# Optimization experiments

Measured on AMD Instinct MI355X. Metric: run time of the kernel, lower is better.

## Reference

```python
import jax, jax.numpy as jnp
import numpy as np

D_MODEL = 96
D_INNER = 192        # expand_factor * d_model
D_STATE = 16
DT_RANK = 6          # ceil(d_model / 16)
D_CONV = 4
N_LAYERS = 2
EPS = 1e-5


def conv3d(x, w, b=None, padding=((0, 0), (0, 0), (0, 0)), groups=1):
    # x: (N, C, L, H, W), w: (O, C//groups, kL, kH, kW)
    y = jax.lax.conv_general_dilated(
        x, w, window_strides=(1, 1, 1), padding=padding,
        dimension_numbers=('NCDHW', 'OIDHW', 'NCDHW'),
        feature_group_count=groups)
    return y if b is None else y + b[None, :, None, None, None]


def rmsnorm(x, w):
    # faithful to source: mean of squares over the LAST dim (W)
    return x * jax.lax.rsqrt(jnp.mean(x * x, axis=-1, keepdims=True) + EPS) * w


def mamba_block(x, p):
    # x: (N, d_model, L, H, W)
    L = x.shape[2]
    xz = conv3d(x, p['in_proj_w'], padding=((0, 0), (1, 1), (1, 1)))
    xi, z = xz[:, :D_INNER], xz[:, D_INNER:]
    # causal depthwise temporal conv: pad d_conv-1, crop to L
    xi = conv3d(xi, p['conv1d_w'], p['conv1d_b'],
                padding=((D_CONV - 1, D_CONV - 1), (0, 0), (0, 0)),
                groups=D_INNER)[:, :, :L]
    xi = jax.nn.silu(xi)
    # --- SSM (selective scan, pscan path) ---
    A = -jnp.exp(p['A_log'])                                   # (K, S)
    dbc = conv3d(xi, p['x_proj_w'])                            # (N, dt_rank+2S, L, H, W)
    delta = jax.nn.softplus(conv3d(dbc[:, :DT_RANK], p['dt_proj_w'], p['dt_proj_b']))  # (N, K, L, H, W)
    B = jnp.moveaxis(dbc[:, DT_RANK:DT_RANK + D_STATE], 1, -1)  # (N, L, H, W, S)
    C = dbc[:, DT_RANK + D_STATE:]                              # (N, S, L, H, W)
    deltaA = jnp.exp(delta[..., None] * A[None, :, None, None, None, :])  # (N,K,L,H,W,S)
    BX = delta[..., None] * B[:, None] * xi[..., None]                    # (N,K,L,H,W,S)

    def op(e1, e2):
        a1, b1 = e1
        a2, b2 = e2
        return a1 * a2, a2 * b1 + b2

    _, hs = jax.lax.associative_scan(op, (deltaA, BX), axis=2)  # scan over L
    y = jnp.einsum('nklhws,nslhw->nklhw', hs, C) + p['D'][None, :, None, None, None] * xi
    out = y * jax.nn.silu(z)
    return conv3d(out, p['out_proj_w'])


def _forward(x, in_proj_w, conv1d_w, conv1d_b, x_proj_w, dt_proj_w,
             dt_proj_b, A_log, D, out_proj_w, norm_w):
    for l in range(N_LAYERS):
        p = dict(in_proj_w=in_proj_w[l], conv1d_w=conv1d_w[l], conv1d_b=conv1d_b[l],
                 x_proj_w=x_proj_w[l], dt_proj_w=dt_proj_w[l], dt_proj_b=dt_proj_b[l],
                 A_log=A_log[l], D=D[l], out_proj_w=out_proj_w[l], norm_w=norm_w[l])
        x = mamba_block(rmsnorm(x, p['norm_w']), p) + x   # ResidualBlock
        x = x[:, :, 0:1]                                   # Mamba.forward keeps t=0 only
    return x


def setup_inputs() -> dict:
    key = jax.random.key(0)
    ks = jax.random.split(key, 12)
    Lk = N_LAYERS
    x = jax.random.normal(ks[0], (2, D_MODEL, 8, 24, 24), dtype=jnp.float32)
    in_proj_w = jax.random.normal(ks[1], (Lk, 2 * D_INNER, D_MODEL, 1, 3, 3), jnp.float32) * (D_MODEL * 9) ** -0.5
    conv1d_w = jax.random.normal(ks[2], (Lk, D_INNER, 1, D_CONV, 1, 1), jnp.float32) * D_CONV ** -0.5
    conv1d_b = jax.random.normal(ks[3], (Lk, D_INNER), jnp.float32) * 0.02
    x_proj_w = jax.random.normal(ks[4], (Lk, DT_RANK + 2 * D_STATE, D_INNER, 1, 1, 1), jnp.float32) * D_INNER ** -0.5
    dt_std = DT_RANK ** -0.5
    dt_proj_w = jax.random.uniform(ks[5], (Lk, D_INNER, DT_RANK, 1, 1, 1), jnp.float32, -dt_std, dt_std)
    # dt bias init: inv softplus of dt ~ LogUniform(dt_min, dt_max)
    dt = jnp.exp(jax.random.uniform(ks[6], (Lk, D_INNER), jnp.float32)
                 * (np.log(0.1) - np.log(0.001)) + np.log(0.001))
    dt = jnp.clip(dt, 1e-4, None)
    dt_proj_b = dt + jnp.log(-jnp.expm1(-dt))
    A_log = jnp.log(jnp.tile(jnp.arange(1, D_STATE + 1, dtype=jnp.float32), (Lk, D_INNER, 1)))
    D = jnp.ones((Lk, D_INNER), jnp.float32)
    out_proj_w = jax.random.normal(ks[7], (Lk, D_MODEL, D_INNER, 1, 1, 1), jnp.float32) * D_INNER ** -0.5
    norm_w = jnp.ones((Lk, 1, D_MODEL, 1, 1, 1), jnp.float32)
    return {'x': x, 'in_proj_w': in_proj_w, 'conv1d_w': conv1d_w, 'conv1d_b': conv1d_b,
            'x_proj_w': x_proj_w, 'dt_proj_w': dt_proj_w, 'dt_proj_b': dt_proj_b,
            'A_log': A_log, 'D': D, 'out_proj_w': out_proj_w, 'norm_w': norm_w}


def reference(x, in_proj_w, conv1d_w, conv1d_b, x_proj_w, dt_proj_w,
              dt_proj_b, A_log, D, out_proj_w, norm_w):
    return _forward(x, in_proj_w, conv1d_w, conv1d_b, x_proj_w, dt_proj_w,
                    dt_proj_b, A_log, D, out_proj_w, norm_w)
```

## Files before the change

### kernel.cpp

```cpp
#include <hip/hip_runtime.h>
#include <math.h>

#define NB   2
#define CM   96
#define CI   192
#define CO   384
#define HP   24
#define WP   24
#define PX   576
#define DTR  6
#define NDBC 38
#define CSPLIT 8
#define CCH  12

__device__ __forceinline__ float siluf(float x){ return x / (1.f + expf(-x)); }
__device__ __forceinline__ float softplusf(float x){ return x > 20.f ? x : log1pf(expf(x)); }
__device__ __forceinline__ unsigned short f2bf(float f){
    unsigned u = __float_as_uint(f);
    return (unsigned short)((u + 0x7fffu + ((u >> 16) & 1u)) >> 16);
}
__device__ __forceinline__ float bflo(unsigned u){ return __uint_as_float(u << 16); }
__device__ __forceinline__ float bfhi(unsigned u){ return __uint_as_float(u & 0xffff0000u); }

#define NW_IN (2*CO*CM*9)
#define WQB_L (CM*CO*8)
#define WRB_L (CM*CO)
#define WPT_L (CI*CM)
__global__ void prep_k(const float* __restrict__ ipw, const float* __restrict__ opw,
                       unsigned short* __restrict__ wQb, unsigned short* __restrict__ wRb,
                       float* __restrict__ wpT){
    int idx = blockIdx.x*256 + threadIdx.x;
    if (idx < NW_IN){
        int l = idx / (CO*CM*9);
        int r = idx % (CO*CM*9);
        int o = r / (CM*9);
        int r2 = r % (CM*9);
        int c = r2 / 9;
        int k = r2 % 9;
        unsigned short v = f2bf(ipw[idx]);
        if (k < 8) wQb[(long)l*WQB_L + ((c*CO + o)<<3) + k] = v;
        else       wRb[(long)l*WRB_L + c*CO + o] = v;
    } else {
        int j = idx - NW_IN;
        if (j < 2*CI*CM){
            int l = j / (CI*CM);
            int r = j % (CI*CM);
            int c = r / CM;
            int m = r % CM;
            wpT[l*WPT_L + c*CM + m] = opw[(l*CM + m)*CI + c];
        }
    }
}

__global__ __launch_bounds__(256) void conv_k(
    const float* __restrict__ x, long nStr, long cStr,
    const float* __restrict__ nw,
    const unsigned short* __restrict__ wQb, const unsigned short* __restrict__ wRb,
    float* __restrict__ acc)
{
    __shared__ float hs[CCH][3][28];
    __shared__ float scl[CCH][3];
    int bx = blockIdx.x;
    int og = blockIdx.y;
    int cs = blockIdx.z;
    int n  = bx / HP, hh = bx % HP;
    int tid = threadIdx.x;
    int c0 = cs*CCH;

    if (tid < CCH*3){
        int c = tid/3, j = tid%3;
        int row = hh + j - 1;
        float s = 0.f;
        if (row >= 0 && row < HP){
            const float* xp = x + (long)n*nStr + (long)(c0+c)*cStr + row*WP;
            #pragma unroll
            for (int w = 0; w < WP; w++){ float v = xp[w]; s += v*v; }
            s = rsqrtf(s*(1.0f/WP) + 1e-5f) * nw[c0+c];
        }
        scl[c][j] = s;
    }
    __syncthreads();

    for (int idx = tid; idx < CCH*3*28; idx += 256){
        int c = idx/84; int rem = idx%84; int j = rem/28; int wc = rem%28;
        int row = hh + j - 1;
        float v = 0.f;
        if (row >= 0 && row < HP && wc >= 1 && wc <= WP)
            v = x[(long)n*nStr + (long)(c0+c)*cStr + row*WP + (wc-1)] * scl[c][j];
        hs[c][j][wc] = v;
    }
    __syncthreads();

    int ol = tid & 63;
    int o  = og*64 + ol;
    int x0 = (tid >> 6) * 6;
    float a0[6] = {0,0,0,0,0,0};
    const uint4* wq4 = (const uint4*)wQb;

    for (int c = 0; c < CCH; c++){
        int cg = c0 + c;
        uint4 wv = wq4[cg*CO + o];
        float w0 = bflo(wv.x), w1 = bfhi(wv.x);
        float w2 = bflo(wv.y), w3 = bfhi(wv.y);
        float w4 = bflo(wv.z), w5 = bfhi(wv.z);
        float w6 = bflo(wv.w), w7 = bfhi(wv.w);
        float w8 = bflo((unsigned)wRb[cg*CO + o]);
        float r0v[8], r1v[8], r2v[8];
        #pragma unroll
        for (int i = 0; i < 4; i++){
            float2 p0 = *(const float2*)(&hs[c][0][x0] + 2*i);
            float2 p1 = *(const float2*)(&hs[c][1][x0] + 2*i);
            float2 p2 = *(const float2*)(&hs[c][2][x0] + 2*i);
            r0v[2*i] = p0.x; r0v[2*i+1] = p0.y;
            r1v[2*i] = p1.x; r1v[2*i+1] = p1.y;
            r2v[2*i] = p2.x; r2v[2*i+1] = p2.y;
        }
        #pragma unroll
        for (int p = 0; p < 6; p++){
            a0[p] += w0*r0v[p] + w1*r0v[p+1] + w2*r0v[p+2]
                   + w3*r1v[p] + w4*r1v[p+1] + w5*r1v[p+2]
                   + w6*r2v[p] + w7*r2v[p+1] + w8*r2v[p+2];
        }
    }

    float* ap = acc + ((long)(cs*NB + n)*PX + hh*WP + x0)*CO + o;
    #pragma unroll
    for (int p = 0; p < 6; p++) ap[p*CO] = a0[p];
}

__global__ __launch_bounds__(256) void ssmproj_k(
    const float* __restrict__ acc,
    const float* __restrict__ c1w, const float* __restrict__ c1b,
    const float* __restrict__ xpw, const float* __restrict__ dtw,
    const float* __restrict__ dtb, const float* __restrict__ Dp,
    const float* __restrict__ wpT,
    const float* __restrict__ xres, long nStrR, long cStrR,
    float* __restrict__ dst)
{
    __shared__ float gl[4][CI];
    int wave = threadIdx.x >> 6, lane = threadIdx.x & 63;
    int p0 = blockIdx.x*4;
    int p  = p0 + wave;
    int n  = p / PX, px = p % PX;

    float xi[3], sz[3];
    #pragma unroll
    for (int t = 0; t < 3; t++){
        int c = lane + 64*t;
        float xr = 0.f, zr = 0.f;
        #pragma unroll
        for (int q = 0; q < CSPLIT; q++){
            const float* ap = acc + ((long)(q*NB + n)*PX + px)*CO;
            xr += ap[c]; zr += ap[CI + c];
        }
        xi[t] = siluf(xr*c1w[c*4 + 3] + c1b[c]);
        sz[t] = siluf(zr);
    }

    float dbc[NDBC];
    #pragma unroll
    for (int j = 0; j < NDBC; j++){
        float s = 0.f;
        #pragma unroll
        for (int t = 0; t < 3; t++) s += xi[t]*xpw[j*CI + lane + 64*t];
        dbc[j] = s;
    }
    #pragma unroll
    for (int step = 1; step < 64; step <<= 1){
        #pragma unroll
        for (int j = 0; j < NDBC; j++) dbc[j] += __shfl_xor(dbc[j], step, 64);
    }
    float BC = 0.f;
    #pragma unroll
    for (int s = 0; s < 16; s++) BC += dbc[6+s]*dbc[22+s];

    #pragma unroll
    for (int t = 0; t < 3; t++){
        int c = lane + 64*t;
        float dl = dtb[c];
        #pragma unroll
        for (int r = 0; r < DTR; r++) dl += dbc[r]*dtw[c*DTR + r];
        dl = softplusf(dl);
        gl[wave][c] = xi[t]*(dl*BC + Dp[c])*sz[t];
    }
    __syncthreads();

    for (int idx = threadIdx.x; idx < 4*CM; idx += 256){
        int pl = idx / CM, m = idx % CM;
        int pp = p0 + pl;
        int nn = pp / PX, ppx = pp % PX;
        const float* g = gl[pl];
        float s0 = 0.f, s1 = 0.f, s2 = 0.f, s3 = 0.f;
        for (int c = 0; c < CI; c += 4){
            s0 += g[c+0]*wpT[(c+0)*CM + m];
            s1 += g[c+1]*wpT[(c+1)*CM + m];
            s2 += g[c+2]*wpT[(c+2)*CM + m];
            s3 += g[c+3]*wpT[(c+3)*CM + m];
        }
        float s = (s0+s1) + (s2+s3);
        s += xres[(long)nn*nStrR + (long)m*cStrR + ppx];
        dst[(nn*CM + m)*PX + ppx] = s;
    }
}

extern "C" void kernel_launch(void* const* d_in, const int* in_sizes, int n_in,
                              void* d_out, int out_size, void* d_ws, size_t ws_size,
                              hipStream_t stream) {
    const float* x_in = (const float*)d_in[0];
    const float* ipw  = (const float*)d_in[1];
    const float* c1w  = (const float*)d_in[2];
    const float* c1b  = (const float*)d_in[3];
    const float* xpw  = (const float*)d_in[4];
    const float* dtw  = (const float*)d_in[5];
    const float* dtb  = (const float*)d_in[6];
    const float* Dp   = (const float*)d_in[8];
    const float* opw  = (const float*)d_in[9];
    const float* nw   = (const float*)d_in[10];

    char* ws = (char*)d_ws;
    unsigned short* wQb = (unsigned short*)ws;
    unsigned short* wRb = wQb + 2*WQB_L;
    float* wpT = (float*)(wRb + 2*WRB_L);
    float* acc = wpT + 2*WPT_L;
    float* x1  = acc + (long)CSPLIT*NB*PX*CO;

    prep_k<<<(NW_IN + 2*CI*CM + 255)/256, 256, 0, stream>>>(ipw, opw, wQb, wRb, wpT);

    conv_k<<<dim3(NB*HP, 6, CSPLIT), 256, 0, stream>>>(
        x_in, 96L*8*PX, 8L*PX, nw, wQb, wRb, acc);
    ssmproj_k<<<NB*PX/4, 256, 0, stream>>>(
        acc, c1w, c1b, xpw, dtw, dtb, Dp, wpT,
        x_in, 96L*8*PX, 8L*PX, x1);

    conv_k<<<dim3(NB*HP, 6, CSPLIT), 256, 0, stream>>>(
        x1, 96L*PX, (long)PX, nw + CM, wQb + WQB_L, wRb + WRB_L, acc);
    ssmproj_k<<<NB*PX/4, 256, 0, stream>>>(
        acc, c1w + CI*4, c1b + CI, xpw + NDBC*CI, dtw + CI*DTR, dtb + CI, Dp + CI, wpT + WPT_L,
        x1, 96L*PX, (long)PX, (float*)d_out);
}
```

Baseline: 162.0 us.

## Fuse all stages into one persistent kernel with grid-wide atomic barriers

Measured after the change: 562.7 us. 247% more time.

```diff
diff --git a/kernel.cpp b/kernel.cpp
--- a/kernel.cpp
+++ b/kernel.cpp
@@ -12,6 +12,15 @@
 #define NDBC 38
 #define CSPLIT 8
 #define CCH  12
+#define NBLK 512
+#define NTHR 256
+#define NVB  (NB*HP*6*CSPLIT)
+
+#define NW_IN (2*CO*CM*9)
+#define WQB_L (CM*CO*8)
+#define WRB_L (CM*CO)
+#define WPT_L (CI*CM)
+#define PREP_TOT (NW_IN + 2*CI*CM)
 
 __device__ __forceinline__ float siluf(float x){ return x / (1.f + expf(-x)); }
 __device__ __forceinline__ float softplusf(float x){ return x > 20.f ? x : log1pf(expf(x)); }
@@ -22,27 +31,204 @@
 __device__ __forceinline__ float bflo(unsigned u){ return __uint_as_float(u << 16); }
 __device__ __forceinline__ float bfhi(unsigned u){ return __uint_as_float(u & 0xffff0000u); }
 
-#define NW_IN (2*CO*CM*9)
-#define WQB_L (CM*CO*8)
-#define WRB_L (CM*CO)
-#define WPT_L (CI*CM)
-__global__ void prep_k(const float* __restrict__ ipw, const float* __restrict__ opw,
-                       unsigned short* __restrict__ wQb, unsigned short* __restrict__ wRb,
-                       float* __restrict__ wpT){
-    int idx = blockIdx.x*256 + threadIdx.x;
-    if (idx < NW_IN){
-        int l = idx / (CO*CM*9);
-        int r = idx % (CO*CM*9);
-        int o = r / (CM*9);
-        int r2 = r % (CM*9);
-        int c = r2 / 9;
-        int k = r2 % 9;
-        unsigned short v = f2bf(ipw[idx]);
-        if (k < 8) wQb[(long)l*WQB_L + ((c*CO + o)<<3) + k] = v;
-        else       wRb[(long)l*WRB_L + c*CO + o] = v;
-    } else {
-        int j = idx - NW_IN;
-        if (j < 2*CI*CM){
+__device__ __forceinline__ void gsync(unsigned* bar, int slot){
+    __syncthreads();
+    __threadfence();
+    if (threadIdx.x == 0){
+        unsigned* sub    = bar + slot*256 + (blockIdx.x & 7)*16;
+        unsigned* master = bar + slot*256 + 128;
+        unsigned old = __hip_atomic_fetch_add(sub, 1u, __ATOMIC_ACQ_REL, __HIP_MEMORY_SCOPE_AGENT);
+        if (old == (unsigned)(NBLK/8 - 1))
+            __hip_atomic_fetch_add(master, 1u, __ATOMIC_ACQ_REL, __HIP_MEMORY_SCOPE_AGENT);
+        while (__hip_atomic_load(master, __ATOMIC_ACQUIRE, __HIP_MEMORY_SCOPE_AGENT) < 8u)
+            __builtin_amdgcn_s_sleep(2);
+    }
+    __syncthreads();
+    __threadfence();
+}
+
+__device__ __forceinline__ void conv_body(
+    int vb, const float* __restrict__ x, long nStr, long cStr,
+    const float* __restrict__ nw,
+    const unsigned short* __restrict__ wQb, const unsigned short* __restrict__ wRb,
+    float* __restrict__ acc, float* __restrict__ hs, float* __restrict__ scl)
+{
+    int bx = vb % (NB*HP);
+    int og = (vb / (NB*HP)) % 6;
+    int cs = vb / (NB*HP*6);
+    int n  = bx / HP, hh = bx % HP;
+    int tid = threadIdx.x;
+    int c0 = cs*CCH;
+
+    if (tid < CCH*3){
+        int c = tid/3, j = tid%3;
+        int row = hh + j - 1;
+        float s = 0.f;
+        if (row >= 0 && row < HP){
+            const float4* xp4 = (const float4*)(x + (long)n*nStr + (long)(c0+c)*cStr + row*WP);
+            #pragma unroll
+            for (int w4 = 0; w4 < WP/4; w4++){
+                float4 v = xp4[w4];
+                s += v.x*v.x + v.y*v.y + v.z*v.z + v.w*v.w;
+            }
+            s = rsqrtf(s*(1.0f/WP) + 1e-5f) * nw[c0+c];
+        }
+        scl[c*3 + j] = s;
+    }
+    __syncthreads();
+
+    for (int idx = tid; idx < CCH*3*28; idx += NTHR){
+        int c = idx/84; int rem = idx%84; int j = rem/28; int wc = rem%28;
+        int row = hh + j - 1;
+        float v = 0.f;
+        if (row >= 0 && row < HP && wc >= 1 && wc <= WP)
+            v = x[(long)n*nStr + (long)(c0+c)*cStr + row*WP + (wc-1)] * scl[c*3 + j];
+        hs[idx] = v;
+    }
+    __syncthreads();
+
+    int ol = tid & 63;
+    int o  = og*64 + ol;
+    int x0 = (tid >> 6) * 6;
+    float a0[6] = {0,0,0,0,0,0};
+    const uint4* wq4 = (const uint4*)wQb;
+
+    for (int c = 0; c < CCH; c++){
+        int cg = c0 + c;
+        uint4 wq = wq4[cg*CO + o];
+        float w0 = bflo(wq.x), w1 = bfhi(wq.x);
+        float w2 = bflo(wq.y), w3 = bfhi(wq.y);
+        float w4 = bflo(wq.z), w5 = bfhi(wq.z);
+        float w6 = bflo(wq.w), w7 = bfhi(wq.w);
+        float w8 = bflo((unsigned)wRb[cg*CO + o]);
+        const float* h0 = hs + (c*3 + 0)*28 + x0;
+        const float* h1 = hs + (c*3 + 1)*28 + x0;
+        const float* h2 = hs + (c*3 + 2)*28 + x0;
+        float r0v[8], r1v[8], r2v[8];
+        #pragma unroll
+        for (int i = 0; i < 4; i++){
+            float2 p0 = *(const float2*)(h0 + 2*i);
+            float2 p1 = *(const float2*)(h1 + 2*i);
+            float2 p2 = *(const float2*)(h2 + 2*i);
+            r0v[2*i] = p0.x; r0v[2*i+1] = p0.y;
+            r1v[2*i] = p1.x; r1v[2*i+1] = p1.y;
+            r2v[2*i] = p2.x; r2v[2*i+1] = p2.y;
+        }
+        #pragma unroll
+        for (int p = 0; p < 6; p++){
+            a0[p] += w0*r0v[p] + w1*r0v[p+1] + w2*r0v[p+2]
+                   + w3*r1v[p] + w4*r1v[p+1] + w5*r1v[p+2]
+                   + w6*r2v[p] + w7*r2v[p+1] + w8*r2v[p+2];
+        }
+    }
+
+    float* ap = acc + ((long)(cs*NB + n)*PX + hh*WP + x0)*CO + o;
+    #pragma unroll
+    for (int p = 0; p < 6; p++) ap[p*CO] = a0[p];
+}
+
+__device__ __forceinline__ void ssm_body(
+    int gw, const float* __restrict__ acc,
+    const float* __restrict__ c1w, const float* __restrict__ c1b,
+    const float* __restrict__ xpw, const float* __restrict__ dtw,
+    const float* __restrict__ dtb, const float* __restrict__ Dp,
+    const float* __restrict__ wpT,
+    const float* __restrict__ xres, long nStrR, long cStrR,
+    float* __restrict__ dst, float* __restrict__ glw)
+{
+    int lane = threadIdx.x & 63;
+    int n = gw / PX, px = gw % PX;
+
+    float xi[3], sz[3];
+    #pragma unroll
+    for (int t = 0; t < 3; t++){
+        int c = lane + 64*t;
+        float xr = 0.f, zr = 0.f;
+        #pragma unroll
+        for (int q = 0; q < CSPLIT; q++){
+            const float* ap = acc + ((long)(q*NB + n)*PX + px)*CO;
+            xr += ap[c]; zr += ap[CI + c];
+        }
+        xi[t] = siluf(xr*c1w[c*4 + 3] + c1b[c]);
+        sz[t] = siluf(zr);
+    }
+
+    float dbc[NDBC];
+    #pragma unroll
+    for (int j = 0; j < NDBC; j++){
+        float s = 0.f;
+        #pragma unroll
+        for (int t = 0; t < 3; t++) s += xi[t]*xpw[j*CI + lane + 64*t];
+        dbc[j] = s;
+    }
+    #pragma unroll
+    for (int step = 1; step < 64; step <<= 1){
+        #pragma unroll
+        for (int j = 0; j < NDBC; j++) dbc[j] += __shfl_xor(dbc[j], step, 64);
+    }
+    float BC = 0.f;
+    #pragma unroll
+    for (int si = 0; si < 16; si++) BC += dbc[6+si]*dbc[22+si];
+
+    #pragma unroll
+    for (int t = 0; t < 3; t++){
+        int c = lane + 64*t;
+        float dl = dtb[c];
+        #pragma unroll
+        for (int r = 0; r < DTR; r++) dl += dbc[r]*dtw[c*DTR + r];
+        dl = softplusf(dl);
+        glw[c] = xi[t]*(dl*BC + Dp[c])*sz[t];
+    }
+    asm volatile("s_waitcnt lgkmcnt(0)" ::: "memory");
+
+    #pragma unroll
+    for (int mi = 0; mi < 2; mi++){
+        int m = mi*64 + lane;
+        if (m < CM){
+            float s0 = 0.f, s1 = 0.f, s2 = 0.f, s3 = 0.f;
+            for (int c = 0; c < CI; c += 4){
+                const float4 g4 = *(const float4*)(glw + c);
+                s0 += g4.x*wpT[(c+0)*CM + m];
+                s1 += g4.y*wpT[(c+1)*CM + m];
+                s2 += g4.z*wpT[(c+2)*CM + m];
+                s3 += g4.w*wpT[(c+3)*CM + m];
+            }
+            float s = (s0+s1) + (s2+s3);
+            s += xres[(long)n*nStrR + (long)m*cStrR + px];
+            dst[(n*CM + m)*PX + px] = s;
+        }
+    }
+}
+
+__global__ __launch_bounds__(NTHR, 2) void mono_k(
+    const float* __restrict__ x_in,
+    const float* __restrict__ ipw,  const float* __restrict__ c1w,
+    const float* __restrict__ c1b,  const float* __restrict__ xpw,
+    const float* __restrict__ dtw,  const float* __restrict__ dtb,
+    const float* __restrict__ Dp,   const float* __restrict__ opw,
+    const float* __restrict__ nw,
+    unsigned* __restrict__ bar,
+    unsigned short* __restrict__ wQb, unsigned short* __restrict__ wRb,
+    float* __restrict__ wpT, float* __restrict__ acc,
+    float* __restrict__ x1, float* __restrict__ dout)
+{
+    __shared__ float smem[CCH*3*28 + CCH*3];
+    const int tid = threadIdx.x;
+    const int bid = blockIdx.x;
+
+    for (int idx = bid*NTHR + tid; idx < PREP_TOT; idx += NBLK*NTHR){
+        if (idx < NW_IN){
+            int l = idx / (CO*CM*9);
+            int r = idx % (CO*CM*9);
+            int o = r / (CM*9);
+            int r2 = r % (CM*9);
+            int c = r2 / 9;
+            int k = r2 % 9;
+            unsigned short v = f2bf(ipw[idx]);
+            if (k < 8) wQb[(long)l*WQB_L + ((c*CO + o)<<3) + k] = v;
+            else       wRb[(long)l*WRB_L + c*CO + o] = v;
+        } else {
+            int j = idx - NW_IN;
             int l = j / (CI*CM);
             int r = j % (CI*CM);
             int c = r / CM;
@@ -50,156 +236,34 @@
             wpT[l*WPT_L + c*CM + m] = opw[(l*CM + m)*CI + c];
         }
     }
-}
-
-__global__ __launch_bounds__(256) void conv_k(
-    const float* __restrict__ x, long nStr, long cStr,
-    const float* __restrict__ nw,
-    const unsigned short* __restrict__ wQb, const unsigned short* __restrict__ wRb,
-    float* __restrict__ acc)
-{
-    __shared__ float hs[CCH][3][28];
-    __shared__ float scl[CCH][3];
-    int bx = blockIdx.x;
-    int og = blockIdx.y;
-    int cs = blockIdx.z;
-    int n  = bx / HP, hh = bx % HP;
-    int tid = threadIdx.x;
-    int c0 = cs*CCH;
-
-    if (tid < CCH*3){
-        int c = tid/3, j = tid%3;
-        int row = hh + j - 1;
-        float s = 0.f;
-        if (row >= 0 && row < HP){
-            const float* xp = x + (long)n*nStr + (long)(c0+c)*cStr + row*WP;
-            #pragma unroll
-            for (int w = 0; w < WP; w++){ float v = xp[w]; s += v*v; }
-            s = rsqrtf(s*(1.0f/WP) + 1e-5f) * nw[c0+c];
-        }
-        scl[c][j] = s;
-    }
-    __syncthreads();
-
-    for (int idx = tid; idx < CCH*3*28; idx += 256){
-        int c = idx/84; int rem = idx%84; int j = rem/28; int wc = rem%28;
-        int row = hh + j - 1;
-        float v = 0.f;
-        if (row >= 0 && row < HP && wc >= 1 && wc <= WP)
-            v = x[(long)n*nStr + (long)(c0+c)*cStr + row*WP + (wc-1)] * scl[c][j];
-        hs[c][j][wc] = v;
-    }
-    __syncthreads();
-
-    int ol = tid & 63;
-    int o  = og*64 + ol;
-    int x0 = (tid >> 6) * 6;
-    float a0[6] = {0,0,0,0,0,0};
-    const uint4* wq4 = (const uint4*)wQb;
-
-    for (int c = 0; c < CCH; c++){
-        int cg = c0 + c;
-        uint4 wv = wq4[cg*CO + o];
-        float w0 = bflo(wv.x), w1 = bfhi(wv.x);
-        float w2 = bflo(wv.y), w3 = bfhi(wv.y);
-        float w4 = bflo(wv.z), w5 = bfhi(wv.z);
-        float w6 = bflo(wv.w), w7 = bfhi(wv.w);
-        float w8 = bflo((unsigned)wRb[cg*CO + o]);
-        float r0v[8], r1v[8], r2v[8];
-        #pragma unroll
-        for (int i = 0; i < 4; i++){
-            float2 p0 = *(const float2*)(&hs[c][0][x0] + 2*i);
-            float2 p1 = *(const float2*)(&hs[c][1][x0] + 2*i);
-            float2 p2 = *(const float2*)(&hs[c][2][x0] + 2*i);
-            r0v[2*i] = p0.x; r0v[2*i+1] = p0.y;
-            r1v[2*i] = p1.x; r1v[2*i+1] = p1.y;
-            r2v[2*i] = p2.x; r2v[2*i+1] = p2.y;
-        }
-        #pragma unroll
-        for (int p = 0; p < 6; p++){
-            a0[p] += w0*r0v[p] + w1*r0v[p+1] + w2*r0v[p+2]
-                   + w3*r1v[p] + w4*r1v[p+1] + w5*r1v[p+2]
-                   + w6*r2v[p] + w7*r2v[p+1] + w8*r2v[p+2];
-        }
-    }
-
-    float* ap = acc + ((long)(cs*NB + n)*PX + hh*WP + x0)*CO + o;
-    #pragma unroll
-    for (int p = 0; p < 6; p++) ap[p*CO] = a0[p];
-}
-
-__global__ __launch_bounds__(256) void ssmproj_k(
-    const float* __restrict__ acc,
-    const float* __restrict__ c1w, const float* __restrict__ c1b,
-    const float* __restrict__ xpw, const float* __restrict__ dtw,
-    const float* __restrict__ dtb, const float* __restrict__ Dp,
-    const float* __restrict__ wpT,
-    const float* __restrict__ xres, long nStrR, long cStrR,
-    float* __restrict__ dst)
-{
-    __shared__ float gl[4][CI];
-    int wave = threadIdx.x >> 6, lane = threadIdx.x & 63;
-    int p0 = blockIdx.x*4;
-    int p  = p0 + wave;
-    int n  = p / PX, px = p % PX;
-
-    float xi[3], sz[3];
-    #pragma unroll
-    for (int t = 0; t < 3; t++){
-        int c = lane + 64*t;
-        float xr = 0.f, zr = 0.f;
-        #pragma unroll
-        for (int q = 0; q < CSPLIT; q++){
-            const float* ap = acc + ((long)(q*NB + n)*PX + px)*CO;
-            xr += ap[c]; zr += ap[CI + c];
-        }
-        xi[t] = siluf(xr*c1w[c*4 + 3] + c1b[c]);
-        sz[t] = siluf(zr);
-    }
-
-    float dbc[NDBC];
-    #pragma unroll
-    for (int j = 0; j < NDBC; j++){
-        float s = 0.f;
-        #pragma unroll
-        for (int t = 0; t < 3; t++) s += xi[t]*xpw[j*CI + lane + 64*t];
-        dbc[j] = s;
-    }
-    #pragma unroll
-    for (int step = 1; step < 64; step <<= 1){
-        #pragma unroll
-        for (int j = 0; j < NDBC; j++) dbc[j] += __shfl_xor(dbc[j], step, 64);
-    }
-    float BC = 0.f;
-    #pragma unroll
-    for (int s = 0; s < 16; s++) BC += dbc[6+s]*dbc[22+s];
-
-    #pragma unroll
-    for (int t = 0; t < 3; t++){
-        int c = lane + 64*t;
-        float dl = dtb[c];
-        #pragma unroll
-        for (int r = 0; r < DTR; r++) dl += dbc[r]*dtw[c*DTR + r];
-        dl = softplusf(dl);
-        gl[wave][c] = xi[t]*(dl*BC + Dp[c])*sz[t];
-    }
-    __syncthreads();
-
-    for (int idx = threadIdx.x; idx < 4*CM; idx += 256){
-        int pl = idx / CM, m = idx % CM;
-        int pp = p0 + pl;
-        int nn = pp / PX, ppx = pp % PX;
-        const float* g = gl[pl];
-        float s0 = 0.f, s1 = 0.f, s2 = 0.f, s3 = 0.f;
-        for (int c = 0; c < CI; c += 4){
-            s0 += g[c+0]*wpT[(c+0)*CM + m];
-            s1 += g[c+1]*wpT[(c+1)*CM + m];
-            s2 += g[c+2]*wpT[(c+2)*CM + m];
-            s3 += g[c+3]*wpT[(c+3)*CM + m];
-        }
-        float s = (s0+s1) + (s2+s3);
-        s += xres[(long)nn*nStrR + (long)m*cStrR + ppx];
-        dst[(nn*CM + m)*PX + ppx] = s;
+    gsync(bar, 0);
+
+    for (int vb = bid; vb < NVB; vb += NBLK)
+        conv_body(vb, x_in, 96L*8*PX, 8L*PX, nw, wQb, wRb, acc,
+                  smem, smem + CCH*3*28);
+    gsync(bar, 1);
+
+    {
+        int wv = tid >> 6;
+        int gw = wv*NBLK + bid;
+        if (gw < NB*PX)
+            ssm_body(gw, acc, c1w, c1b, xpw, dtw, dtb, Dp, wpT,
+                     x_in, 96L*8*PX, 8L*PX, x1, smem + wv*CI);
+    }
+    gsync(bar, 2);
+
+    for (int vb = bid; vb < NVB; vb += NBLK)
+        conv_body(vb, x1, 96L*PX, (long)PX, nw + CM, wQb + WQB_L, wRb + WRB_L, acc,
+                  smem, smem + CCH*3*28);
+    gsync(bar, 3);
+
+    {
+        int wv = tid >> 6;
+        int gw = wv*NBLK + bid;
+        if (gw < NB*PX)
+            ssm_body(gw, acc, c1w + CI*4, c1b + CI, xpw + NDBC*CI, dtw + CI*DTR,
+                     dtb + CI, Dp + CI, wpT + WPT_L,
+                     x1, 96L*PX, (long)PX, dout, smem + wv*CI);
     }
 }
 
@@ -218,23 +282,16 @@
     const float* nw   = (const float*)d_in[10];
 
     char* ws = (char*)d_ws;
-    unsigned short* wQb = (unsigned short*)ws;
+    unsigned* bar = (unsigned*)ws;
+    unsigned short* wQb = (unsigned short*)(ws + 4096);
     unsigned short* wRb = wQb + 2*WQB_L;
     float* wpT = (float*)(wRb + 2*WRB_L);
     float* acc = wpT + 2*WPT_L;
     float* x1  = acc + (long)CSPLIT*NB*PX*CO;
 
-    prep_k<<<(NW_IN + 2*CI*CM + 255)/256, 256, 0, stream>>>(ipw, opw, wQb, wRb, wpT);
-
-    conv_k<<<dim3(NB*HP, 6, CSPLIT), 256, 0, stream>>>(
-        x_in, 96L*8*PX, 8L*PX, nw, wQb, wRb, acc);
-    ssmproj_k<<<NB*PX/4, 256, 0, stream>>>(
-        acc, c1w, c1b, xpw, dtw, dtb, Dp, wpT,
-        x_in, 96L*8*PX, 8L*PX, x1);
-
-    conv_k<<<dim3(NB*HP, 6, CSPLIT), 256, 0, stream>>>(
-        x1, 96L*PX, (long)PX, nw + CM, wQb + WQB_L, wRb + WRB_L, acc);
-    ssmproj_k<<<NB*PX/4, 256, 0, stream>>>(
-        acc, c1w + CI*4, c1b + CI, xpw + NDBC*CI, dtw + CI*DTR, dtb + CI, Dp + CI, wpT + WPT_L,
-        x1, 96L*PX, (long)PX, (float*)d_out);
-}
+    hipMemsetAsync(bar, 0, 4096, stream);
+
+    mono_k<<<NBLK, NTHR, 0, stream>>>(
+        x_in, ipw, c1w, c1b, xpw, dtw, dtb, Dp, opw, nw,
+        bar, wQb, wRb, wpT, acc, x1, (float*)d_out);
+}
```
